# Performance work log

Hardware: AMD Instinct MI355X
Metric: run time of the kernel (lower is better)

The kernel has to match this reference:

```python
import jax, jax.numpy as jnp
import numpy as np

HEADS = 8
DH_QK = 32
DH_V = 32
BS = 8          # block_size
HALO = 3
WIN = BS + 2 * HALO  # 14
REL = 2 * WIN - 1    # 27
SCALE = DH_QK ** -0.5


def setup_inputs() -> dict:
    key = jax.random.key(0)
    k1, k2, k3, k4, k5 = jax.random.split(key, 5)
    dim = 256
    dim_out_qk = HEADS * DH_QK  # 256
    dim_out_v = HEADS * DH_V    # 256
    std = dim ** -0.5
    x = jax.random.normal(k1, (4, dim, 128, 128), jnp.float32)
    w_q = jax.random.normal(k2, (dim_out_qk, dim), jnp.float32) * std
    w_kv = jax.random.normal(k3, (dim_out_qk + dim_out_v, dim), jnp.float32) * std
    height_rel = jax.random.normal(k4, (REL, DH_QK), jnp.float32) * SCALE
    width_rel = jax.random.normal(k5, (REL, DH_QK), jnp.float32) * SCALE
    return {"x": x, "w_q": w_q, "w_kv": w_kv, "height_rel": height_rel, "width_rel": width_rel}


def rel_logits_1d(q, rel_k, permute):
    N, H, W, d = q.shape
    rel_size = rel_k.shape[0]
    win = (rel_size + 1) // 2
    x = jnp.einsum('nhwd,rd->nhwr', q, rel_k)
    x = x.reshape(-1, W, rel_size)
    x = jnp.pad(x, ((0, 0), (0, 0), (0, 1))).reshape(x.shape[0], -1)
    x = jnp.pad(x, ((0, 0), (0, rel_size - W)))
    x = x.reshape(-1, W + 1, rel_size)
    x = x[:, :W, win - 1:]
    x = x.reshape(N, H, 1, W, win)
    x = jnp.broadcast_to(x, (N, H, win, W, win))
    return x.transpose(permute)


def pos_embed_rel(q, height_rel, width_rel):
    # q: (BH, nblocks, bs*bs, dh)
    B, BB, HW, dh = q.shape
    qb = q.reshape(-1, BS, BS, dh)
    rel_w = rel_logits_1d(qb, width_rel, (0, 1, 3, 2, 4))
    rel_h = rel_logits_1d(qb.transpose(0, 2, 1, 3), height_rel, (0, 3, 1, 4, 2))
    return (rel_h + rel_w).reshape(B, BB, HW, -1)


def reference(x, w_q, w_kv, height_rel, width_rel):
    B, C, H, W = x.shape
    nh, nw = H // BS, W // BS
    nb = nh * nw
    # 1x1 conv projections as einsum
    q = jnp.einsum('bchw,oc->bohw', x, w_q)
    # (B*heads, nb, bs*bs, dh_qk), queries row-major within block, blocks row-major
    q = q.reshape(B * HEADS, DH_QK, nh, BS, nw, BS).transpose(0, 2, 4, 3, 5, 1)
    q = q.reshape(B * HEADS, nb, BS * BS, DH_QK)
    kv = jnp.einsum('bchw,oc->bohw', x, w_kv)
    kv = jnp.pad(kv, ((0, 0), (0, 0), (HALO, HALO), (HALO, HALO)))
    # halo windows via gather (unfold)
    ih = np.arange(nh)[:, None] * BS + np.arange(WIN)[None, :]
    iw = np.arange(nw)[:, None] * BS + np.arange(WIN)[None, :]
    kv = kv[:, :, ih]
    kv = kv[:, :, :, :, iw]
    kv = kv.transpose(0, 1, 2, 4, 3, 5)
    kv = kv.reshape(B * HEADS, DH_QK + DH_V, nb, WIN * WIN).transpose(0, 2, 3, 1)
    k = kv[..., :DH_QK]
    v = kv[..., DH_QK:]
    attn = jnp.einsum('bnqd,bnkd->bnqk', q, k) * SCALE + pos_embed_rel(q, height_rel, width_rel)
    attn = jax.nn.softmax(attn, axis=-1)
    out = jnp.einsum('bnqk,bnkd->bnqd', attn, v)
    # (BH, nb, HW, dv) -> (B, heads*dv, H, W)
    out = out.transpose(0, 3, 2, 1)  # (BH, dv, HW, nb)
    out = out.reshape(-1, BS, BS, nh, nw).transpose(0, 3, 1, 4, 2)
    out = out.reshape(B, HEADS * DH_V, H, W)
    return out
```

## Files before the change

kernel.cpp:

```cpp
#include <hip/hip_runtime.h>
#include <hip/hip_bf16.h>
#include <stdint.h>

#define HEADS 8
#define DH    32
#define BSZ   8
#define HALO  3
#define WIN   14
#define NKEY  196
#define CIN   256
#define IMG   128
#define HWPIX 16384
#define MQKV  768
#define SCALE 0.17677669529663689f

#define KS_STRIDE 36
#define VT_STRIDE 228
#define PQ_STRIDE 112
#define QB_STRIDE 64

#define BST_STRIDE 264
#define AS_STRIDE  68

typedef short bf16x8 __attribute__((ext_vector_type(8)));
typedef short bf16x4 __attribute__((ext_vector_type(4)));
typedef float f32x4  __attribute__((ext_vector_type(4)));
typedef unsigned short u16x4 __attribute__((ext_vector_type(4)));
typedef unsigned short u16x8 __attribute__((ext_vector_type(8)));

#define AS1 __attribute__((address_space(1)))
#define AS3 __attribute__((address_space(3)))

__device__ __forceinline__ float bf2f(unsigned short s){ return __uint_as_float(((unsigned int)s) << 16); }
__device__ __forceinline__ unsigned short f2bf(float f){
  unsigned int u = __float_as_uint(f);
  u += 0x7fffu + ((u >> 16) & 1u);
  return (unsigned short)(u >> 16);
}

__device__ __forceinline__ ushort2 pk2c(float a, float b) {
  __hip_bfloat162 h = __float22bfloat162_rn(make_float2(a, b));
  union { __hip_bfloat162 h2; ushort2 v; } r; r.h2 = h; return r.v;
}
__device__ __forceinline__ void st_bf4c(unsigned short* p, f32x4 c) {
  ushort2 lo = pk2c(c[0], c[1]), hi = pk2c(c[2], c[3]);
  ushort4 o; o.x = lo.x; o.y = lo.y; o.z = hi.x; o.w = hi.y;
  *(ushort4*)p = o;
}

__device__ __forceinline__ bf16x8 ld2(const unsigned short* p) {
  bf16x4 a = *(const bf16x4*)p;
  bf16x4 b = *(const bf16x4*)(p + 4);
  bf16x8 r;
  r[0]=a[0]; r[1]=a[1]; r[2]=a[2]; r[3]=a[3];
  r[4]=b[0]; r[5]=b[1]; r[6]=b[2]; r[7]=b[3];
  return r;
}

__device__ __forceinline__ void st_bf4(unsigned short* p, f32x4 c) {
  ushort4 o;
  o.x = f2bf(c[0]); o.y = f2bf(c[1]); o.z = f2bf(c[2]); o.w = f2bf(c[3]);
  *(ushort4*)p = o;
}

__global__ void convw_kernel(const float* __restrict__ wq,
                             const float* __restrict__ wkv,
                             unsigned short* __restrict__ Wb)
{
  int idx = blockIdx.x * 256 + threadIdx.x;
  int m = idx >> 6, c4 = idx & 63;
  int h = m / 96, d = m - h * 96;
  const float* src = (d < 32) ? wq  + (size_t)(h * 32 + d) * CIN
                              : wkv + (size_t)(h * 64 + d - 32) * CIN;
  float4 v = *(const float4*)(src + c4 * 4);
  ushort4 o;
  o.x = f2bf(v.x); o.y = f2bf(v.y); o.z = f2bf(v.z); o.w = f2bf(v.w);
  *(ushort4*)(Wb + (size_t)m * CIN + c4 * 4) = o;
}

__global__ void convrel_kernel(const float* __restrict__ hrel,
                               const float* __restrict__ wrel,
                               unsigned short* __restrict__ relb)
{
  int idx = blockIdx.x * 256 + threadIdx.x;
  int r = idx >> 5, c = idx & 31;
  float v = 0.f;
  if (r < 27) v = hrel[r * 32 + c];
  else if (r >= 32 && r < 59) v = wrel[(r - 32) * 32 + c];
  relb[idx] = f2bf(v);
}

__global__ __launch_bounds__(256, 3)
void projx_kernel(const float* __restrict__ x,
                  const unsigned short* __restrict__ Wb,
                  unsigned short* __restrict__ qkv)
{
  __shared__ unsigned short Bst[64 * BST_STRIDE];
  __shared__ unsigned short As[128 * AS_STRIDE];

  const int tid = threadIdx.x;
  const int w = tid >> 6, lane = tid & 63;
  const int g16 = lane >> 4, l15 = lane & 15;
  const int p0 = blockIdx.x * 64;
  const int bl = blockIdx.y;
  const int wm = w >> 1, wn = w & 1;
  const float* xin = x + (size_t)bl * CIN * HWPIX;

  const int arow = lane >> 3;
  const int acol = (lane & 7) * 8;

  bf16x8 areg[4];
  #pragma unroll
  for (int c = 0; c < 4; ++c) {
    int ci = w * 4 + c;
    areg[c] = *(const bf16x8*)(Wb + (size_t)(ci * 8 + arow) * CIN + acol);
  }

  for (int idx = tid; idx < 2048; idx += 256) {
    int cp = idx >> 4, f = idx & 15;
    const float* r0 = xin + (size_t)(2 * cp) * HWPIX + p0 + f * 4;
    float4 a = *(const float4*)r0;
    float4 b = *(const float4*)(r0 + HWPIX);
    unsigned short* bp = Bst + (f * 4) * BST_STRIDE + cp * 2;
    *(ushort2*)(bp                 ) = pk2c(a.x, b.x);
    *(ushort2*)(bp + BST_STRIDE    ) = pk2c(a.y, b.y);
    *(ushort2*)(bp + BST_STRIDE * 2) = pk2c(a.z, b.z);
    *(ushort2*)(bp + BST_STRIDE * 3) = pk2c(a.w, b.w);
  }
  __syncthreads();

  for (int mt = 0; mt < 6; ++mt) {
    f32x4 acc[4][2];
    #pragma unroll
    for (int i = 0; i < 4; ++i)
      #pragma unroll
      for (int j = 0; j < 2; ++j) acc[i][j] = (f32x4){0.f,0.f,0.f,0.f};

    #pragma unroll
    for (int kk = 0; kk < 4; ++kk) {
      #pragma unroll
      for (int c = 0; c < 4; ++c) {
        int ci = w * 4 + c;
        *(bf16x8*)(As + (ci * 8 + arow) * AS_STRIDE + acol) = areg[c];
      }
      __syncthreads();

      {
        int nit = mt * 4 + kk + 1;
        if (nit < 24) {
          int nm0 = (nit >> 2) * 128, nk0 = (nit & 3) * 64;
          #pragma unroll
          for (int c = 0; c < 4; ++c) {
            int ci = w * 4 + c;
            areg[c] = *(const bf16x8*)(Wb + (size_t)(nm0 + ci * 8 + arow) * CIN + nk0 + acol);
          }
        }
      }

      const int k0 = kk * 64;
      #pragma unroll
      for (int kh = 0; kh < 2; ++kh) {
        bf16x8 af[4], bfr[2];
        #pragma unroll
        for (int t = 0; t < 4; ++t)
          af[t] = *(const bf16x8*)(As + (wm*64 + t*16 + l15) * AS_STRIDE + kh*32 + g16*8);
        #pragma unroll
        for (int t = 0; t < 2; ++t)
          bfr[t] = *(const bf16x8*)(Bst + (wn*32 + t*16 + l15)*BST_STRIDE + k0 + kh*32 + g16*8);
        #pragma unroll
        for (int tm = 0; tm < 4; ++tm)
          #pragma unroll
          for (int tn = 0; tn < 2; ++tn)
            acc[tm][tn] = __builtin_amdgcn_mfma_f32_16x16x32_bf16(
                            af[tm], bfr[tn], acc[tm][tn], 0, 0, 0);
      }
      __syncthreads();
    }

    const int m0 = mt * 128;
    #pragma unroll
    for (int tm = 0; tm < 4; ++tm) {
      int ch = wm*64 + tm*16 + g16*4;
      #pragma unroll
      for (int tn = 0; tn < 2; ++tn) {
        int pix = wn*32 + tn*16 + l15;
        unsigned int boff = (unsigned)(pix*256 + ((ch*2) ^ ((l15 & 7) << 4)));
        st_bf4c((unsigned short*)((char*)As + boff), acc[tm][tn]);
      }
    }
    __syncthreads();
    {
      unsigned short* qrow = qkv + ((size_t)bl * HWPIX + p0) * MQKV + m0;
      #pragma unroll
      for (int r = 0; r < 4; ++r) {
        int pl = w*16 + r*4 + g16;
        unsigned int boff = (unsigned)(pl*256 + ((l15*16) ^ ((pl & 7) << 4)));
        u16x8 vv = *(const u16x8*)((const char*)As + boff);
        *(u16x8*)(qrow + (size_t)pl * MQKV + l15*8) = vv;
      }
    }
    __syncthreads();
  }
}

__global__ __launch_bounds__(256, 3)
void attn_kernel(const unsigned short* __restrict__ qkv,
                 const unsigned short* __restrict__ relb,
                 float* __restrict__ out,
                 int b0)
{
  __shared__ unsigned short Ks[224 * KS_STRIDE];
  __shared__ unsigned short Vt[32 * VT_STRIDE];
  __shared__ unsigned short Pq[64 * PQ_STRIDE];
  __shared__ unsigned short QB[64 * QB_STRIDE];

  const int tid = threadIdx.x;
  const int by = blockIdx.x >> 4, bx = blockIdx.x & 15;
  const int hd = blockIdx.y, bb = blockIdx.z;
  const size_t pixbase = (size_t)bb * HWPIX;

  const int w = tid >> 6, lane = tid & 63;
  const int g16 = lane >> 4, l15 = lane & 15;
  const int q = w * 16 + l15;
  const int qy = q >> 3, qx = q & 7;
  const int gy = by * BSZ + qy, gx = bx * BSZ + qx;
  const int rot = qx * 4;

  bf16x8 qf = *(const bf16x8*)(qkv + (pixbase + (size_t)gy * IMG + gx) * MQKV + hd * 96 + g16 * 8);

  *(uint4*)(Pq + tid * 8) = *(const uint4*)(relb + tid * 8);

  for (int idx = tid; idx < 224 * 8; idx += 256) {
    int key = idx >> 3, part = idx & 7;
    int ky = key >> 4, kx = key & 15;
    int sy = by * BSZ - HALO + ky, sx = bx * BSZ - HALO + kx;
    uint4 val = make_uint4(0,0,0,0);
    if (kx < WIN && (unsigned)sy < (unsigned)IMG && (unsigned)sx < (unsigned)IMG)
      val = *(const uint4*)(qkv + (pixbase + sy * IMG + sx) * MQKV + hd * 96 + 32 + part * 8);
    if (part < 4) {
      unsigned short* kp = Ks + key * KS_STRIDE + part * 8;
      *(unsigned long long*)(kp    ) = (unsigned long long)val.x | ((unsigned long long)val.y << 32);
      *(unsigned long long*)(kp + 4) = (unsigned long long)val.z | ((unsigned long long)val.w << 32);
    } else {
      int dh0 = (part - 4) * 8;
      unsigned int u[4] = {val.x, val.y, val.z, val.w};
      #pragma unroll
      for (int e = 0; e < 4; ++e) {
        Vt[(dh0 + 2*e    ) * VT_STRIDE + key] = (unsigned short)(u[e] & 0xffffu);
        Vt[(dh0 + 2*e + 1) * VT_STRIDE + key] = (unsigned short)(u[e] >> 16);
      }
    }
  }
  __syncthreads();

  {
    const unsigned short* Hb = Pq;
    const unsigned short* Wr = Pq + 1024;
    bf16x8 ah0 = *(const bf16x8*)(Hb + l15 * 32 + g16 * 8);
    bf16x8 ah1 = *(const bf16x8*)(Hb + (16 + l15) * 32 + g16 * 8);
    bf16x8 aw0 = *(const bf16x8*)(Wr + l15 * 32 + g16 * 8);
    bf16x8 aw1 = *(const bf16x8*)(Wr + (16 + l15) * 32 + g16 * 8);
    f32x4 z = (f32x4){0.f,0.f,0.f,0.f};
    f32x4 ch0 = __builtin_amdgcn_mfma_f32_16x16x32_bf16(ah0, qf, z, 0, 0, 0);
    f32x4 ch1 = __builtin_amdgcn_mfma_f32_16x16x32_bf16(ah1, qf, z, 0, 0, 0);
    f32x4 cw0 = __builtin_amdgcn_mfma_f32_16x16x32_bf16(aw0, qf, z, 0, 0, 0);
    f32x4 cw1 = __builtin_amdgcn_mfma_f32_16x16x32_bf16(aw1, qf, z, 0, 0, 0);
    unsigned short* QBq = QB + q * QB_STRIDE;
    st_bf4c(QBq +      (( 0 + g16 * 4 + rot) & 31), ch0);
    st_bf4c(QBq +      ((16 + g16 * 4 + rot) & 31), ch1);
    st_bf4c(QBq + 32 + (( 0 + g16 * 4 + rot) & 31), cw0);
    st_bf4c(QBq + 32 + ((16 + g16 * 4 + rot) & 31), cw1);
  }
  __syncthreads();

  const unsigned short* QBq = QB + q * QB_STRIDE;
  unsigned short* Prow = Pq + q * PQ_STRIDE;

  const float LOG2E = 1.4426950408889634f;
  const float SL2E  = SCALE * LOG2E;

  float bw2[4];
  #pragma unroll
  for (int i = 0; i < 4; ++i) {
    int kx = g16 * 4 + i;
    bw2[i] = (kx < WIN) ? bf2f(QBq[32 + ((kx - qx + 13 + rot) & 31)]) * LOG2E : -1e30f;
  }
  const int hbase = 13 - qy + rot;

  float lsum = 0.f;
  f32x4 o0 = (f32x4){0.f,0.f,0.f,0.f}, o1 = (f32x4){0.f,0.f,0.f,0.f};
  const f32x4 z = (f32x4){0.f,0.f,0.f,0.f};

  #pragma unroll
  for (int half = 0; half < 2; ++half) {
    #pragma unroll
    for (int u = 0; u < 7; ++u) {
      const int nt = half * 7 + u;
      bf16x8 kf = ld2(Ks + (nt * 16 + l15) * KS_STRIDE + g16 * 8);
      f32x4 c = __builtin_amdgcn_mfma_f32_16x16x32_bf16(kf, qf, z, 0, 0, 0);
      float bh2 = bf2f(QBq[(nt + hbase) & 31]) * LOG2E;
      float p0 = exp2f(fmaf(c[0], SL2E, bh2 + bw2[0]));
      float p1 = exp2f(fmaf(c[1], SL2E, bh2 + bw2[1]));
      float p2 = exp2f(fmaf(c[2], SL2E, bh2 + bw2[2]));
      float p3 = exp2f(fmaf(c[3], SL2E, bh2 + bw2[3]));
      lsum += (p0 + p1) + (p2 + p3);
      unsigned int plo, phi;
      asm("v_cvt_pk_bf16_f32 %0, %1, %2" : "=v"(plo) : "v"(p0), "v"(p1));
      asm("v_cvt_pk_bf16_f32 %0, %1, %2" : "=v"(phi) : "v"(p2), "v"(p3));
      union { unsigned int u32[2]; u16x4 v; } pk_;
      pk_.u32[0] = plo; pk_.u32[1] = phi;
      *(u16x4*)(Prow + u * 16 + g16 * 4) = pk_.v;
    }
    asm volatile("" ::: "memory");
    #pragma unroll
    for (int cc = 0; cc < 4; ++cc) {
      bf16x8 pf = (bf16x8){0,0,0,0,0,0,0,0};
      const bool masked = (cc == 3);
      if (!masked || g16 < 2)
        pf = *(const bf16x8*)(Prow + cc * 32 + g16 * 8);
      int vcol = half * 112 + cc * 32 + g16 * 8;
      if (masked && g16 >= 2) vcol = 0;
      bf16x8 v0 = ld2(Vt + l15 * VT_STRIDE + vcol);
      bf16x8 v1 = ld2(Vt + (16 + l15) * VT_STRIDE + vcol);
      o0 = __builtin_amdgcn_mfma_f32_16x16x32_bf16(v0, pf, o0, 0, 0, 0);
      o1 = __builtin_amdgcn_mfma_f32_16x16x32_bf16(v1, pf, o1, 0, 0, 0);
    }
  }

  lsum += __shfl_xor(lsum, 16);
  lsum += __shfl_xor(lsum, 32);
  float inv = 1.f / lsum;

  float* ob = out + (((size_t)(b0 + bb) * 256 + hd * DH) * HWPIX) + (size_t)gy * IMG + gx;
  #pragma unroll
  for (int i = 0; i < 4; ++i) {
    int dh0 = g16 * 4 + i;
    ob[(size_t)dh0 * HWPIX]        = o0[i] * inv;
    ob[(size_t)(dh0 + 16) * HWPIX] = o1[i] * inv;
  }
}

extern "C" void kernel_launch(void* const* d_in, const int* in_sizes, int n_in,
                              void* d_out, int out_size, void* d_ws, size_t ws_size,
                              hipStream_t stream)
{
  (void)in_sizes; (void)n_in; (void)out_size;
  const float* x    = (const float*)d_in[0];
  const float* wq   = (const float*)d_in[1];
  const float* wkv  = (const float*)d_in[2];
  const float* hrel = (const float*)d_in[3];
  const float* wrel = (const float*)d_in[4];
  float* out = (float*)d_out;

  const size_t wb_bytes   = (size_t)MQKV * CIN * 2;
  const size_t relb_bytes = 4096;
  const size_t qkv_per_b  = (size_t)HWPIX * MQKV * 2;
  const int chunk = (ws_size >= wb_bytes + relb_bytes + 4 * qkv_per_b) ? 4 : 1;

  unsigned short* Wb   = (unsigned short*)d_ws;
  unsigned short* relb = (unsigned short*)((char*)d_ws + wb_bytes);
  unsigned short* qkv  = (unsigned short*)((char*)d_ws + wb_bytes + relb_bytes);

  convw_kernel<<<192, 256, 0, stream>>>(wq, wkv, Wb);
  convrel_kernel<<<8, 256, 0, stream>>>(hrel, wrel, relb);

  for (int b0 = 0; b0 < 4; b0 += chunk) {
    projx_kernel<<<dim3(256, chunk), 256, 0, stream>>>(x + (size_t)b0 * CIN * HWPIX, Wb, qkv);
    attn_kernel<<<dim3(256, HEADS, chunk), 256, 0, stream>>>(qkv, relb, out, b0);
  }
}
```

Before: 246.1 us.

## Redistribute softmax probabilities via lane shuffles instead of LDS staging buffer

Removes the Pq shared-memory buffer for probabilities. Each lane keeps its packed bf16 P values in registers, and the B-operand fragment for the PV MFMA is assembled with cross-lane __shfl calls. The relative-embedding staging reuses the QB buffer, guarded by an extra barrier. The LDS saving allows raising launch bounds to 4 blocks per CU, at the cost of many ds_bpermute shuffles plus selects and higher register pressure.

```diff
diff --git a/kernel.cpp b/kernel.cpp
--- a/kernel.cpp
+++ b/kernel.cpp
@@ -16,7 +16,6 @@
 
 #define KS_STRIDE 36
 #define VT_STRIDE 228
-#define PQ_STRIDE 112
 #define QB_STRIDE 64
 
 #define BST_STRIDE 264
@@ -55,12 +54,6 @@
   r[0]=a[0]; r[1]=a[1]; r[2]=a[2]; r[3]=a[3];
   r[4]=b[0]; r[5]=b[1]; r[6]=b[2]; r[7]=b[3];
   return r;
-}
-
-__device__ __forceinline__ void st_bf4(unsigned short* p, f32x4 c) {
-  ushort4 o;
-  o.x = f2bf(c[0]); o.y = f2bf(c[1]); o.z = f2bf(c[2]); o.w = f2bf(c[3]);
-  *(ushort4*)p = o;
 }
 
 __global__ void convw_kernel(const float* __restrict__ wq,
@@ -203,7 +196,7 @@
   }
 }
 
-__global__ __launch_bounds__(256, 3)
+__global__ __launch_bounds__(256, 4)
 void attn_kernel(const unsigned short* __restrict__ qkv,
                  const unsigned short* __restrict__ relb,
                  float* __restrict__ out,
@@ -211,7 +204,6 @@
 {
   __shared__ unsigned short Ks[224 * KS_STRIDE];
   __shared__ unsigned short Vt[32 * VT_STRIDE];
-  __shared__ unsigned short Pq[64 * PQ_STRIDE];
   __shared__ unsigned short QB[64 * QB_STRIDE];
 
   const int tid = threadIdx.x;
@@ -228,7 +220,7 @@
 
   bf16x8 qf = *(const bf16x8*)(qkv + (pixbase + (size_t)gy * IMG + gx) * MQKV + hd * 96 + g16 * 8);
 
-  *(uint4*)(Pq + tid * 8) = *(const uint4*)(relb + tid * 8);
+  *(uint4*)(QB + tid * 8) = *(const uint4*)(relb + tid * 8);
 
   for (int idx = tid; idx < 224 * 8; idx += 256) {
     int key = idx >> 3, part = idx & 7;
@@ -254,12 +246,13 @@
   __syncthreads();
 
   {
-    const unsigned short* Hb = Pq;
-    const unsigned short* Wr = Pq + 1024;
+    const unsigned short* Hb = QB;
+    const unsigned short* Wr = QB + 1024;
     bf16x8 ah0 = *(const bf16x8*)(Hb + l15 * 32 + g16 * 8);
     bf16x8 ah1 = *(const bf16x8*)(Hb + (16 + l15) * 32 + g16 * 8);
     bf16x8 aw0 = *(const bf16x8*)(Wr + l15 * 32 + g16 * 8);
     bf16x8 aw1 = *(const bf16x8*)(Wr + (16 + l15) * 32 + g16 * 8);
+    __syncthreads();
     f32x4 z = (f32x4){0.f,0.f,0.f,0.f};
     f32x4 ch0 = __builtin_amdgcn_mfma_f32_16x16x32_bf16(ah0, qf, z, 0, 0, 0);
     f32x4 ch1 = __builtin_amdgcn_mfma_f32_16x16x32_bf16(ah1, qf, z, 0, 0, 0);
@@ -274,7 +267,6 @@
   __syncthreads();
 
   const unsigned short* QBq = QB + q * QB_STRIDE;
-  unsigned short* Prow = Pq + q * PQ_STRIDE;
 
   const float LOG2E = 1.4426950408889634f;
   const float SL2E  = SCALE * LOG2E;
@@ -287,12 +279,17 @@
   }
   const int hbase = 13 - qy + rot;
 
+  const int srcA = l15 + ((g16 & 1) ? 32 : 0);
+  const int srcB = srcA + 16;
+  const bool hiTile = (g16 >> 1) != 0;
+
   float lsum = 0.f;
   f32x4 o0 = (f32x4){0.f,0.f,0.f,0.f}, o1 = (f32x4){0.f,0.f,0.f,0.f};
   const f32x4 z = (f32x4){0.f,0.f,0.f,0.f};
 
   #pragma unroll
   for (int half = 0; half < 2; ++half) {
+    unsigned int Plo[7], Phi[7];
     #pragma unroll
     for (int u = 0; u < 7; ++u) {
       const int nt = half * 7 + u;
@@ -307,17 +304,24 @@
       unsigned int plo, phi;
       asm("v_cvt_pk_bf16_f32 %0, %1, %2" : "=v"(plo) : "v"(p0), "v"(p1));
       asm("v_cvt_pk_bf16_f32 %0, %1, %2" : "=v"(phi) : "v"(p2), "v"(p3));
-      union { unsigned int u32[2]; u16x4 v; } pk_;
-      pk_.u32[0] = plo; pk_.u32[1] = phi;
-      *(u16x4*)(Prow + u * 16 + g16 * 4) = pk_.v;
-    }
-    asm volatile("" ::: "memory");
+      Plo[u] = plo; Phi[u] = phi;
+    }
     #pragma unroll
     for (int cc = 0; cc < 4; ++cc) {
-      bf16x8 pf = (bf16x8){0,0,0,0,0,0,0,0};
+      const int ua = 2 * cc;
+      const int ub = (cc < 3) ? (2 * cc + 1) : 6;
+      unsigned int a0 = __shfl(Plo[ua], srcA, 64), a1 = __shfl(Phi[ua], srcA, 64);
+      unsigned int b0 = __shfl(Plo[ub], srcA, 64), b1 = __shfl(Phi[ub], srcA, 64);
+      unsigned int c0 = __shfl(Plo[ua], srcB, 64), c1 = __shfl(Phi[ua], srcB, 64);
+      unsigned int d0 = __shfl(Plo[ub], srcB, 64), d1 = __shfl(Phi[ub], srcB, 64);
+      union { unsigned int u32[4]; bf16x8 v; } pfu;
+      pfu.u32[0] = hiTile ? b0 : a0;
+      pfu.u32[1] = hiTile ? b1 : a1;
+      pfu.u32[2] = hiTile ? d0 : c0;
+      pfu.u32[3] = hiTile ? d1 : c1;
+      bf16x8 pf = pfu.v;
       const bool masked = (cc == 3);
-      if (!masked || g16 < 2)
-        pf = *(const bf16x8*)(Prow + cc * 32 + g16 * 8);
+      if (masked && g16 >= 2) pf = (bf16x8){0,0,0,0,0,0,0,0};
       int vcol = half * 112 + cc * 32 + g16 * 8;
       if (masked && g16 >= 2) vcol = 0;
       bf16x8 v0 = ld2(Vt + l15 * VT_STRIDE + vcol);
```

Measured after the change: 242.1 us. No clear change (-1.6%).
